# Kernel tuning notes

Measured on AMD Instinct MI355X. Metric: run time of the kernel, lower is better.

The kernel has to match this reference:

```python
import jax, jax.numpy as jnp
import numpy as np

N_NODES = 100000
N_NBRS = 16
D_IN = 512
D_EGO = 32
D_LOCAL = 32
D_GLOBAL = 32


def setup_inputs() -> dict:
    key = jax.random.key(0)
    ks = jax.random.split(key, 12)
    x = jax.random.uniform(ks[0], (N_NODES, D_IN), dtype=jnp.float32)
    # adj_list: row 0 = source (neighbor) node, row 1 = destination node.
    # score_local_sparse reshapes to [N, n, d_local], so dst must be each node
    # index repeated N_NBRS times, in order.
    src = jax.random.randint(ks[1], (N_NODES * N_NBRS,), 0, N_NODES, dtype=jnp.int32)
    dst = jnp.repeat(jnp.arange(N_NODES, dtype=jnp.int32), N_NBRS)
    adj_list = jnp.stack([src, dst], axis=0)
    return {
        "adj_list": adj_list,
        "x": x,
        "qk_ego_w": jax.random.normal(ks[2], (D_EGO, D_IN), dtype=jnp.float32) * 0.04,
        "v_ego_w": jax.random.normal(ks[3], (D_IN, D_EGO), dtype=jnp.float32) - 2.0,
        "q_local_w": jax.random.normal(ks[4], (D_LOCAL, D_IN), dtype=jnp.float32) / 10.0 - 2.0,
        "k_local_w": jax.random.normal(ks[5], (D_LOCAL, D_IN), dtype=jnp.float32) / 10.0 - 2.0,
        "v_local_w": jax.random.normal(ks[6], (D_IN, D_LOCAL), dtype=jnp.float32) / 10.0 - 2.0,
        "q_global_w": jax.random.normal(ks[7], (D_GLOBAL, D_IN), dtype=jnp.float32) / 10.0 - 2.0,
        "k_global_w": jax.random.normal(ks[8], (D_GLOBAL, D_IN), dtype=jnp.float32) / 10.0 - 2.0,
        "v_global_w": jax.random.normal(ks[9], (D_IN, D_GLOBAL), dtype=jnp.float32) / 10.0 - 2.0,
        "bias_b": jnp.zeros((1, D_IN), dtype=jnp.float32),
    }


def _nonneg(w):
    return jax.nn.elu(w) + 1.0


def _norm_nonneg(w):
    t = jax.nn.sigmoid(w)
    return t / t.sum()


def reference(adj_list, x, qk_ego_w, v_ego_w, q_local_w, k_local_w, v_local_w,
              q_global_w, k_global_w, v_global_w, bias_b):
    n_cells, d_in = x.shape
    inv = 1.0 / d_in
    inv2 = inv * inv

    # ego branch: plain linear, squared scores
    ego_emb = x @ qk_ego_w.T                      # [N, d_ego]
    ego_scores = (ego_emb * inv) ** 2             # [N, d_ego]

    # local branch: gather-based bilinear scores over k-NN graph
    q_loc = x @ _norm_nonneg(q_local_w).T         # [N, d_local]
    k_loc = x @ _nonneg(k_local_w).T              # [N, d_local]
    prod = q_loc[adj_list[1]] * k_loc[adj_list[0]]  # [E, d_local]
    n_nbr = prod.shape[0] // n_cells
    local_scores = prod.reshape(n_cells, n_nbr, -1) * inv2  # [N, n, d_local]
    exp_local = local_scores.sum(axis=1)          # [N, d_local] (sum over neighbors)

    # global branch: bilinear with mean cell x_bar
    x_bar = x.mean(axis=0, keepdims=True)         # [1, d_in]
    q_glob = x @ _norm_nonneg(q_global_w).T       # [N, d_global]
    k_glob = x_bar @ _nonneg(k_global_w).T        # [1, d_global]
    exp_global = q_glob * k_glob * inv2           # [N, d_global]

    sum_exp = (0.001
               + ego_scores.sum(axis=-1, keepdims=True)
               + exp_local.sum(axis=-1, keepdims=True)
               + exp_global.sum(axis=-1, keepdims=True))  # [N, 1]

    ego_res = (ego_scores / sum_exp) @ _nonneg(v_ego_w).T       # [N, d_out]
    local_res = (exp_local / sum_exp) @ _nonneg(v_local_w).T    # [N, d_out]
    global_res = (exp_global / sum_exp) @ _nonneg(v_global_w).T # [N, d_out]

    res = ego_res + local_res + global_res + (jax.nn.elu(bias_b) + 1.0)
    return res
```

## Files before the change

kernel.cpp:

```cpp
#include <hip/hip_runtime.h>
#include <hip/hip_bf16.h>
#include <math.h>

#define NNODES 100000
#define NNBRS  16
#define NBLK   ((NNODES + 127) / 128)
#define XCG    512

typedef short  s16x8 __attribute__((ext_vector_type(8)));
typedef ushort u16x8 __attribute__((ext_vector_type(8)));
typedef float  f32x4 __attribute__((ext_vector_type(4)));

__device__ __forceinline__ float nonneg_(float w) { return w > 0.f ? w + 1.f : __expf(w); }
__device__ __forceinline__ float sigmoid_(float w) { return 1.f / (1.f + __expf(-w)); }
__device__ __forceinline__ ushort f2b(float f) {
    unsigned u = __builtin_bit_cast(unsigned, f);
    return (ushort)((u + 0x7FFFu + ((u >> 16) & 1u)) >> 16);
}
__device__ __forceinline__ float b2f(ushort h) {
    return __builtin_bit_cast(float, (unsigned)h << 16);
}
__device__ __forceinline__ short fbh(float f) {
    __hip_bfloat16 h = __float2bfloat16(f);
    return __builtin_bit_cast(short, h);
}
__device__ __forceinline__ s16x8 cvt8(float4 lo, float4 hi) {
    s16x8 r;
    r[0] = fbh(lo.x); r[1] = fbh(lo.y); r[2] = fbh(lo.z); r[3] = fbh(lo.w);
    r[4] = fbh(hi.x); r[5] = fbh(hi.y); r[6] = fbh(hi.z); r[7] = fbh(hi.w);
    return r;
}

#define BAR() do {                                             \
    __builtin_amdgcn_sched_barrier(0);                         \
    asm volatile("s_waitcnt lgkmcnt(0)" ::: "memory");         \
    __builtin_amdgcn_sched_barrier(0);                         \
    __builtin_amdgcn_s_barrier();                              \
    __builtin_amdgcn_sched_barrier(0);                         \
} while (0)

__global__ __launch_bounds__(256) void k_sumsig(const float* __restrict__ qlw,
                                                const float* __restrict__ qgw,
                                                float* __restrict__ sums) {
    __shared__ float rr[8];
    const int tid = threadIdx.x, lane = tid & 63, wv = tid >> 6;
    const int base = blockIdx.x * 512;
    float s0 = sigmoid_(qlw[base + tid]) + sigmoid_(qlw[base + 256 + tid]);
    float s1 = sigmoid_(qgw[base + tid]) + sigmoid_(qgw[base + 256 + tid]);
#pragma unroll
    for (int o = 32; o > 0; o >>= 1) {
        s0 += __shfl_down(s0, o);
        s1 += __shfl_down(s1, o);
    }
    if (lane == 0) { rr[wv] = s0; rr[4 + wv] = s1; }
    __syncthreads();
    if (tid == 0) atomicAdd(&sums[0], rr[0] + rr[1] + rr[2] + rr[3]);
    if (tid == 1) atomicAdd(&sums[1], rr[4] + rr[5] + rr[6] + rr[7]);
}

__global__ __launch_bounds__(256) void k_xcast(const float* __restrict__ x,
                                               ushort* __restrict__ x_bf,
                                               float* __restrict__ xcs) {
    __shared__ float csred[4][512];
    const int t = threadIdx.x;
    const int NCH = (NNODES * 512) / 8;
    float a[8] = {0.f,0.f,0.f,0.f,0.f,0.f,0.f,0.f};
    for (int cid = blockIdx.x * 256 + t; cid < NCH; cid += XCG * 256 * 4) {
#pragma unroll
        for (int c4 = 0; c4 < 4; c4++) {
            int cc = cid + c4 * XCG * 256;
            if (cc < NCH) {
                size_t f = (size_t)cc * 8;
                float4 lo = *(const float4*)(x + f);
                float4 hi = *(const float4*)(x + f + 4);
                *(s16x8*)(x_bf + f) = cvt8(lo, hi);
                a[0]+=lo.x; a[1]+=lo.y; a[2]+=lo.z; a[3]+=lo.w;
                a[4]+=hi.x; a[5]+=hi.y; a[6]+=hi.z; a[7]+=hi.w;
            }
        }
    }
    const int c0 = (t * 8) & 511, slice = t >> 6;
#pragma unroll
    for (int j = 0; j < 8; j++) csred[slice][c0 + j] = a[j];
    __syncthreads();
    {
        const int c1 = t, c2 = t + 256;
        float s1 = csred[0][c1] + csred[1][c1] + csred[2][c1] + csred[3][c1];
        float s2 = csred[0][c2] + csred[1][c2] + csred[2][c2] + csred[3][c2];
        xcs[blockIdx.x * 512 + c1] = s1;
        xcs[blockIdx.x * 512 + c2] = s2;
    }
}

__global__ __launch_bounds__(256) void k_prep(const float* __restrict__ qk_ego,
                                              const float* __restrict__ qlw,
                                              const float* __restrict__ klw,
                                              const float* __restrict__ qgw,
                                              const float* __restrict__ ve,
                                              const float* __restrict__ vl,
                                              const float* __restrict__ vg,
                                              const float* __restrict__ bias_b,
                                              ushort* __restrict__ B1t,
                                              ushort* __restrict__ Vt,
                                              float* __restrict__ biasvec) {
    int idx = blockIdx.x * 256 + threadIdx.x;
    if (idx < 128 * 512) {
        int o = idx >> 9, k = idx & 511;
        float v;
        if (o < 32)       v = qk_ego[o * 512 + k];
        else if (o < 64)  v = sigmoid_(qlw[(o - 32) * 512 + k]);
        else if (o < 96)  v = nonneg_(klw[(o - 64) * 512 + k]);
        else              v = sigmoid_(qgw[(o - 96) * 512 + k]);
        B1t[idx] = f2b(v);
    } else if (idx < 128 * 512 + 512 * 96) {
        int j = idx - 128 * 512;
        int d = j / 96, e = j % 96;
        const float* src = (e < 32) ? ve : (e < 64 ? vl : vg);
        Vt[j] = f2b(nonneg_(src[d * 32 + (e & 31)]));
    } else if (idx < 128 * 512 + 512 * 96 + 512) {
        int d = idx - 128 * 512 - 512 * 96;
        float b = bias_b[d];
        biasvec[d] = (b > 0.f ? b + 1.f : __expf(b));
    }
}

__global__ __launch_bounds__(512) void k_proj(const ushort* __restrict__ x_bf,
                                              const ushort* __restrict__ B1t,
                                              ushort* __restrict__ ego_a,
                                              ushort* __restrict__ qloc_a,
                                              ushort* __restrict__ kloc_a,
                                              ushort* __restrict__ qglob_a) {
    __shared__ ushort Bs[128 * 128];
    const int t = threadIdx.x, lane = t & 63, w = t >> 6;
    const int lr = lane & 15, g = lane >> 4;
    const int row0 = blockIdx.x * 128;
    const int myrow = row0 + w * 16 + lr;
    const ushort* xr = x_bf + (size_t)(myrow < NNODES ? myrow : NNODES - 1) * 512
                       + g * 8;
    const char* B1tc = (const char*)B1t;

    uint4 bst[4];
#define BLOAD(seg) { _Pragma("unroll")                                        \
    for (int c = 0; c < 4; c++) {                                             \
        int l = c * 512 + t; int r = l >> 4; int sl = l & 15;                 \
        bst[c] = *(const uint4*)(B1tc + r * 1024 + (seg) * 256 + sl * 16);    \
    } }
#define BWRITE() { _Pragma("unroll")                                          \
    for (int c = 0; c < 4; c++) {                                             \
        int l = c * 512 + t; int r = l >> 4; int sl = l & 15;                 \
        *(uint4*)((char*)Bs + r * 256 + ((sl * 16) ^ ((r & 7) << 4))) =       \
            bst[c];                                                           \
    } }

    f32x4 acc[8];
#pragma unroll
    for (int n = 0; n < 8; n++) acc[n] = (f32x4){0.f, 0.f, 0.f, 0.f};

    s16x8 A0 = *(const s16x8*)(xr);
    s16x8 A1 = *(const s16x8*)(xr + 32);
    s16x8 A2 = *(const s16x8*)(xr + 64);
    s16x8 A3 = *(const s16x8*)(xr + 96);

    BLOAD(0)
    BWRITE()
    BAR();
    BLOAD(1)

#define ASTEP(AR)                                                             \
        af = AR;                                                              \
        if (s + 4 < 16) AR = *(const s16x8*)(xr + (s + 4) * 32);

#pragma unroll
    for (int s = 0; s < 16; s++) {
        const int st = s & 3, seg = s >> 2;
        if (st == 0 && seg > 0) {
            BAR();
            BWRITE();
            BAR();
            if (seg < 3) BLOAD(seg + 1)
        }
        s16x8 af;
        if (st == 0)      { ASTEP(A0) }
        else if (st == 1) { ASTEP(A1) }
        else if (st == 2) { ASTEP(A2) }
        else              { ASTEP(A3) }
#pragma unroll
        for (int n = 0; n < 8; n++) {
            s16x8 bf = *(const s16x8*)((const char*)Bs + (n * 16 + lr) * 256 +
                                       ((st * 64 + g * 16) ^ ((lr & 7) << 4)));
            acc[n] = __builtin_amdgcn_mfma_f32_16x16x32_bf16(af, bf, acc[n], 0, 0, 0);
        }
    }
#undef ASTEP
#undef BLOAD
#undef BWRITE

    __syncthreads();
    char* regn = (char*)Bs + w * 4096;
#pragma unroll
    for (int n = 0; n < 8; n++) {
        const int col = (n >> 1) * 32 + (n & 1) * 16 + lr;
#pragma unroll
        for (int i = 0; i < 4; i++) {
            int row = g * 4 + i;
            *(ushort*)(regn + row * 256 + ((col * 2) ^ ((row & 7) << 4))) =
                f2b(acc[n][i]);
        }
    }
    {
        const int rr = lane & 15, a2 = lane >> 4;
        uint4 v0 = *(const uint4*)(regn + rr * 256 + (( 0 + a2 * 64) ^ ((rr & 7) << 4)));
        uint4 v1 = *(const uint4*)(regn + rr * 256 + ((16 + a2 * 64) ^ ((rr & 7) << 4)));
        uint4 v2 = *(const uint4*)(regn + rr * 256 + ((32 + a2 * 64) ^ ((rr & 7) << 4)));
        uint4 v3 = *(const uint4*)(regn + rr * 256 + ((48 + a2 * 64) ^ ((rr & 7) << 4)));
        int grow = row0 + w * 16 + rr;
        if (grow < NNODES) {
            ushort* ap = (a2 == 0) ? ego_a : (a2 == 1) ? qloc_a
                        : (a2 == 2) ? kloc_a : qglob_a;
            uint4* dp = (uint4*)(ap + (size_t)grow * 32);
            dp[0] = v0; dp[1] = v1; dp[2] = v2; dp[3] = v3;
        }
    }
}

__global__ __launch_bounds__(256) void k_kredA(const float* __restrict__ xcs,
                                               float* __restrict__ csum2) {
    const int t = threadIdx.x, b = blockIdx.x;
    const float* base = xcs + (size_t)b * 8 * 512;
    float s1 = 0.f, s2 = 0.f;
#pragma unroll
    for (int r = 0; r < 8; r++) {
        s1 += base[r * 512 + t];
        s2 += base[r * 512 + 256 + t];
    }
    csum2[(size_t)b * 512 + t] = s1;
    csum2[(size_t)b * 512 + 256 + t] = s2;
}

__global__ __launch_bounds__(256) void k_kredB(const float* __restrict__ csum2,
                                               const float* __restrict__ kgw,
                                               float* __restrict__ kacc) {
    __shared__ float cs[512];
    const int t = threadIdx.x;
    float s0 = 0.f, s1 = 0.f;
    for (int b = 0; b < 64; b++) {
        s0 += csum2[(size_t)b * 512 + t];
        s1 += csum2[(size_t)b * 512 + 256 + t];
    }
    cs[t] = s0; cs[256 + t] = s1;
    __syncthreads();
    const int e = t >> 3, j = t & 7;
    float p = 0.f;
    for (int d = j * 64; d < j * 64 + 64; d++)
        p += cs[d] * nonneg_(kgw[e * 512 + d]);
    p += __shfl_xor(p, 1);
    p += __shfl_xor(p, 2);
    p += __shfl_xor(p, 4);
    if (j == 0) kacc[e] = p;
}

__global__ __launch_bounds__(256, 4) void k_fused(const ushort* __restrict__ ego_a,
                                                  const ushort* __restrict__ qloc_a,
                                                  const ushort* __restrict__ kloc_a,
                                                  const ushort* __restrict__ qglob_a,
                                                  const int* __restrict__ src,
                                                  const float* __restrict__ kacc,
                                                  const float* __restrict__ sums,
                                                  const ushort* __restrict__ Vt,
                                                  const float* __restrict__ biasvec,
                                                  float* __restrict__ out) {
    __shared__ float4 stg4[2048];
    char* stg = (char*)stg4;
    const int t = threadIdx.x, lane = t & 63, w = t >> 6;
    const int lr = lane & 15, g = lane >> 4;
    const int node = blockIdx.x * 64 + w * 16 + lr;
    const int nc = node < NNODES ? node : NNODES - 1;

    const float inv = 1.f / 512.f;
    const float inv2 = inv * inv;
    const float scl = inv2 / sums[0];
    const float scg = inv2 / sums[1] * (1.f / (float)NNODES);
    float kg[8];
    {
        float4 kg0 = *(const float4*)(kacc + g * 8);
        float4 kg1 = *(const float4*)(kacc + g * 8 + 4);
        kg[0]=kg0.x; kg[1]=kg0.y; kg[2]=kg0.z; kg[3]=kg0.w;
        kg[4]=kg1.x; kg[5]=kg1.y; kg[6]=kg1.z; kg[7]=kg1.w;
    }

    s16x8 p0, p1, p2;
    {
        u16x8 e8 = *(const u16x8*)(ego_a   + (size_t)nc * 32 + g * 8);
        u16x8 q8 = *(const u16x8*)(qloc_a  + (size_t)nc * 32 + g * 8);
        u16x8 g8 = *(const u16x8*)(qglob_a + (size_t)nc * 32 + g * 8);
        int4 si0 = *(const int4*)(src + (size_t)nc * 16);
        int4 si1 = *(const int4*)(src + (size_t)nc * 16 + 4);
        int4 si2 = *(const int4*)(src + (size_t)nc * 16 + 8);
        int4 si3 = *(const int4*)(src + (size_t)nc * 16 + 12);
        float ks[8] = {0.f,0.f,0.f,0.f,0.f,0.f,0.f,0.f};
#define GAT(sn) {                                                             \
        u16x8 kv = *(const u16x8*)(kloc_a + (size_t)(sn) * 32 + g * 8);       \
        _Pragma("unroll")                                                     \
        for (int j = 0; j < 8; j++) ks[j] += b2f(kv[j]);                      \
    }
        GAT(si0.x) GAT(si0.y) GAT(si0.z) GAT(si0.w)
        GAT(si1.x) GAT(si1.y) GAT(si1.z) GAT(si1.w)
        GAT(si2.x) GAT(si2.y) GAT(si2.z) GAT(si2.w)
        GAT(si3.x) GAT(si3.y) GAT(si3.z) GAT(si3.w)
#undef GAT
        float se[8], sl[8], sg[8];
        float tt = 0.f;
#pragma unroll
        for (int j = 0; j < 8; j++) {
            float e = b2f(e8[j]) * inv;
            se[j] = e * e;
            sl[j] = b2f(q8[j]) * ks[j] * scl;
            sg[j] = b2f(g8[j]) * kg[j] * scg;
            tt += se[j] + sl[j] + sg[j];
        }
        tt += __shfl_xor(tt, 16);
        tt += __shfl_xor(tt, 32);
        float is = 1.f / (0.001f + tt);
#pragma unroll
        for (int j = 0; j < 8; j++) {
            p0[j] = (short)f2b(se[j] * is);
            p1[j] = (short)f2b(sl[j] * is);
            p2[j] = (short)f2b(sg[j] * is);
        }
    }

    const int srow = w * 16 + lr;
    const int sxor = (srow & 7) << 4;
#pragma unroll
    for (int gi = 0; gi < 4; gi++) {
        if (gi) __syncthreads();
#pragma unroll
        for (int m2 = 0; m2 < 8; m2++) {
            const int m = gi * 8 + m2;
            const ushort* vp = Vt + (size_t)(m * 16 + lr) * 96 + g * 8;
            s16x8 a0 = *(const s16x8*)(vp);
            s16x8 a1 = *(const s16x8*)(vp + 32);
            s16x8 a2 = *(const s16x8*)(vp + 64);
            f32x4 dA = (f32x4){0.f,0.f,0.f,0.f};
            dA = __builtin_amdgcn_mfma_f32_16x16x32_bf16(a0, p0, dA, 0, 0, 0);
            dA = __builtin_amdgcn_mfma_f32_16x16x32_bf16(a1, p1, dA, 0, 0, 0);
            dA = __builtin_amdgcn_mfma_f32_16x16x32_bf16(a2, p2, dA, 0, 0, 0);
            float4 bb = *(const float4*)(biasvec + m * 16 + g * 4);
            float4 o4 = {dA[0]+bb.x, dA[1]+bb.y, dA[2]+bb.z, dA[3]+bb.w};
            *(float4*)(stg + srow * 512 + ((m2 * 64 + g * 16) ^ sxor)) = o4;
        }
        __syncthreads();
#pragma unroll
        for (int k = 0; k < 8; k++) {
            const int lin = k * 1024 + t * 4;
            const int row = lin >> 7, inrow = lin & 127;
            f32x4 v = *(const f32x4*)(stg + row * 512 +
                                      ((inrow * 4) ^ ((row & 7) << 4)));
            const int gnode = blockIdx.x * 64 + row;
            if (gnode < NNODES)
                __builtin_nontemporal_store(
                    v, (f32x4*)(out + (size_t)gnode * 512 + gi * 128 + inrow));
        }
    }
}

extern "C" void kernel_launch(void* const* d_in, const int* in_sizes, int n_in,
                              void* d_out, int out_size, void* d_ws, size_t ws_size,
                              hipStream_t stream) {
    (void)in_sizes; (void)n_in; (void)out_size; (void)ws_size;
    const int*   adj    = (const int*)d_in[0];
    const float* x      = (const float*)d_in[1];
    const float* qk_ego = (const float*)d_in[2];
    const float* v_ego  = (const float*)d_in[3];
    const float* qlw    = (const float*)d_in[4];
    const float* klw    = (const float*)d_in[5];
    const float* vl     = (const float*)d_in[6];
    const float* qgw    = (const float*)d_in[7];
    const float* kgw    = (const float*)d_in[8];
    const float* vg     = (const float*)d_in[9];
    const float* bias_b = (const float*)d_in[10];
    float* out = (float*)d_out;
    float* ws  = (float*)d_ws;

    float*  kacc    = ws;
    float*  sums    = ws + 32;
    float*  biasvec = ws + 64;
    ushort* B1t     = (ushort*)(ws + 1024);
    ushort* Vt      = (ushort*)(ws + 33792);
    ushort* ego_a   = (ushort*)(ws + 65536);
    ushort* qloc_a  = (ushort*)(ws + 65536 + 1600000);
    ushort* kloc_a  = (ushort*)(ws + 65536 + 3200000);
    ushort* qglob_a = (ushort*)(ws + 65536 + 4800000);
    float*  xcs     = ws + 6465536;
    ushort* x_bf    = (ushort*)(ws + 6750208);
    float*  csum2   = ws + 6750208 + 25600000;

    (void)hipMemsetAsync(sums, 0, 2 * sizeof(float), stream);
    k_sumsig<<<32, 256, 0, stream>>>(qlw, qgw, sums);
    k_xcast<<<XCG, 256, 0, stream>>>(x, x_bf, xcs);
    {
        int total = 128 * 512 + 512 * 96 + 512;
        k_prep<<<(total + 255) / 256, 256, 0, stream>>>(qk_ego, qlw, klw, qgw,
                                                        v_ego, vl, vg, bias_b,
                                                        B1t, Vt, biasvec);
    }
    k_proj<<<NBLK, 512, 0, stream>>>(x_bf, B1t, ego_a, qloc_a, kloc_a, qglob_a);
    k_kredA<<<64, 256, 0, stream>>>(xcs, csum2);
    k_kredB<<<1, 256, 0, stream>>>(csum2, kgw, kacc);
    k_fused<<<(NNODES + 63) / 64, 256, 0, stream>>>(ego_a, qloc_a, kloc_a, qglob_a,
                                                    adj, kacc, sums, Vt, biasvec, out);
}
```

Before: 179.8 us.

## Fuse fp32-to-bf16 cast and column sums into projection GEMM kernel

Removes the separate x cast kernel that wrote a full bf16 copy of x and reread it. The projection kernel now loads fp32 x directly, converts it to bf16 into a swizzled LDS tile, and accumulates per-block column sums for the mean. This drops one full write and read of the bf16 intermediate. In exchange it uses more LDS per block, adds extra shuffles, and stages A through LDS with extra barriers, which may lower occupancy.

```diff
diff --git a/kernel.cpp b/kernel.cpp
--- a/kernel.cpp
+++ b/kernel.cpp
@@ -5,7 +5,7 @@
 #define NNODES 100000
 #define NNBRS  16
 #define NBLK   ((NNODES + 127) / 128)
-#define XCG    512
+#define KRA    ((NBLK + 7) / 8)
 
 typedef short  s16x8 __attribute__((ext_vector_type(8)));
 typedef ushort u16x8 __attribute__((ext_vector_type(8)));
@@ -56,40 +56,6 @@
     __syncthreads();
     if (tid == 0) atomicAdd(&sums[0], rr[0] + rr[1] + rr[2] + rr[3]);
     if (tid == 1) atomicAdd(&sums[1], rr[4] + rr[5] + rr[6] + rr[7]);
-}
-
-__global__ __launch_bounds__(256) void k_xcast(const float* __restrict__ x,
-                                               ushort* __restrict__ x_bf,
-                                               float* __restrict__ xcs) {
-    __shared__ float csred[4][512];
-    const int t = threadIdx.x;
-    const int NCH = (NNODES * 512) / 8;
-    float a[8] = {0.f,0.f,0.f,0.f,0.f,0.f,0.f,0.f};
-    for (int cid = blockIdx.x * 256 + t; cid < NCH; cid += XCG * 256 * 4) {
-#pragma unroll
-        for (int c4 = 0; c4 < 4; c4++) {
-            int cc = cid + c4 * XCG * 256;
-            if (cc < NCH) {
-                size_t f = (size_t)cc * 8;
-                float4 lo = *(const float4*)(x + f);
-                float4 hi = *(const float4*)(x + f + 4);
-                *(s16x8*)(x_bf + f) = cvt8(lo, hi);
-                a[0]+=lo.x; a[1]+=lo.y; a[2]+=lo.z; a[3]+=lo.w;
-                a[4]+=hi.x; a[5]+=hi.y; a[6]+=hi.z; a[7]+=hi.w;
-            }
-        }
-    }
-    const int c0 = (t * 8) & 511, slice = t >> 6;
-#pragma unroll
-    for (int j = 0; j < 8; j++) csred[slice][c0 + j] = a[j];
-    __syncthreads();
-    {
-        const int c1 = t, c2 = t + 256;
-        float s1 = csred[0][c1] + csred[1][c1] + csred[2][c1] + csred[3][c1];
-        float s2 = csred[0][c2] + csred[1][c2] + csred[2][c2] + csred[3][c2];
-        xcs[blockIdx.x * 512 + c1] = s1;
-        xcs[blockIdx.x * 512 + c2] = s2;
-    }
 }
 
 __global__ __launch_bounds__(256) void k_prep(const float* __restrict__ qk_ego,
@@ -124,19 +90,21 @@
     }
 }
 
-__global__ __launch_bounds__(512) void k_proj(const ushort* __restrict__ x_bf,
-                                              const ushort* __restrict__ B1t,
-                                              ushort* __restrict__ ego_a,
-                                              ushort* __restrict__ qloc_a,
-                                              ushort* __restrict__ kloc_a,
-                                              ushort* __restrict__ qglob_a) {
+__global__ __launch_bounds__(512, 2) void k_projx(const float* __restrict__ x,
+                                                  const ushort* __restrict__ B1t,
+                                                  ushort* __restrict__ ego_a,
+                                                  ushort* __restrict__ qloc_a,
+                                                  ushort* __restrict__ kloc_a,
+                                                  ushort* __restrict__ qglob_a,
+                                                  float* __restrict__ xcs) {
+    __shared__ ushort As[128 * 128];
     __shared__ ushort Bs[128 * 128];
+    __shared__ float  cs[8][512];
     const int t = threadIdx.x, lane = t & 63, w = t >> 6;
     const int lr = lane & 15, g = lane >> 4;
     const int row0 = blockIdx.x * 128;
-    const int myrow = row0 + w * 16 + lr;
-    const ushort* xr = x_bf + (size_t)(myrow < NNODES ? myrow : NNODES - 1) * 512
-                       + g * 8;
+    const int arow_ = t >> 4;
+    const int acol_ = (t & 15) * 8;
     const char* B1tc = (const char*)B1t;
 
     uint4 bst[4];
@@ -152,50 +120,80 @@
             bst[c];                                                           \
     } }
 
+    float4 al0[4], al1[4];
+#define ALOAD(seg) { _Pragma("unroll")                                        \
+    for (int p = 0; p < 4; p++) {                                             \
+        int rr = p * 32 + arow_;                                              \
+        int grow = row0 + rr; if (grow > NNODES - 1) grow = NNODES - 1;       \
+        const float* sp = x + (size_t)grow * 512 + (seg) * 128 + acol_;       \
+        al0[p] = *(const float4*)(sp);                                        \
+        al1[p] = *(const float4*)(sp + 4);                                    \
+    } }
+#define AWRITE(seg) {                                                         \
+    float a8[8] = {0.f,0.f,0.f,0.f,0.f,0.f,0.f,0.f};                          \
+    _Pragma("unroll")                                                         \
+    for (int p = 0; p < 4; p++) {                                             \
+        int rr = p * 32 + arow_;                                              \
+        if (row0 + rr < NNODES) {                                             \
+            a8[0]+=al0[p].x; a8[1]+=al0[p].y; a8[2]+=al0[p].z; a8[3]+=al0[p].w;\
+            a8[4]+=al1[p].x; a8[5]+=al1[p].y; a8[6]+=al1[p].z; a8[7]+=al1[p].w;\
+        }                                                                     \
+        *(s16x8*)((char*)As + rr * 256 + ((acol_ * 2) ^ ((rr & 7) << 4))) =   \
+            cvt8(al0[p], al1[p]);                                             \
+    }                                                                         \
+    _Pragma("unroll")                                                         \
+    for (int j = 0; j < 8; j++) {                                             \
+        a8[j] += __shfl_xor(a8[j], 16);                                       \
+        a8[j] += __shfl_xor(a8[j], 32);                                       \
+    }                                                                         \
+    if ((lane >> 4) == 0) { _Pragma("unroll")                                 \
+        for (int j = 0; j < 8; j++)                                           \
+            cs[w][(seg) * 128 + lr * 8 + j] = a8[j];                          \
+    } }
+
     f32x4 acc[8];
 #pragma unroll
     for (int n = 0; n < 8; n++) acc[n] = (f32x4){0.f, 0.f, 0.f, 0.f};
 
-    s16x8 A0 = *(const s16x8*)(xr);
-    s16x8 A1 = *(const s16x8*)(xr + 32);
-    s16x8 A2 = *(const s16x8*)(xr + 64);
-    s16x8 A3 = *(const s16x8*)(xr + 96);
-
+    ALOAD(0)
     BLOAD(0)
+    AWRITE(0)
     BWRITE()
     BAR();
-    BLOAD(1)
-
-#define ASTEP(AR)                                                             \
-        af = AR;                                                              \
-        if (s + 4 < 16) AR = *(const s16x8*)(xr + (s + 4) * 32);
-
-#pragma unroll
-    for (int s = 0; s < 16; s++) {
-        const int st = s & 3, seg = s >> 2;
-        if (st == 0 && seg > 0) {
+
+#pragma unroll
+    for (int seg = 0; seg < 4; seg++) {
+        if (seg < 3) { ALOAD(seg + 1) BLOAD(seg + 1) }
+#pragma unroll
+        for (int st = 0; st < 4; st++) {
+            const int ar = w * 16 + lr;
+            s16x8 af = *(const s16x8*)((const char*)As + ar * 256 +
+                                       ((st * 64 + g * 16) ^ ((ar & 7) << 4)));
+#pragma unroll
+            for (int n = 0; n < 8; n++) {
+                s16x8 bf = *(const s16x8*)((const char*)Bs + (n * 16 + lr) * 256 +
+                                           ((st * 64 + g * 16) ^ ((lr & 7) << 4)));
+                acc[n] = __builtin_amdgcn_mfma_f32_16x16x32_bf16(af, bf, acc[n], 0, 0, 0);
+            }
+        }
+        if (seg < 3) {
             BAR();
-            BWRITE();
+            AWRITE(seg + 1)
+            BWRITE()
             BAR();
-            if (seg < 3) BLOAD(seg + 1)
-        }
-        s16x8 af;
-        if (st == 0)      { ASTEP(A0) }
-        else if (st == 1) { ASTEP(A1) }
-        else if (st == 2) { ASTEP(A2) }
-        else              { ASTEP(A3) }
-#pragma unroll
-        for (int n = 0; n < 8; n++) {
-            s16x8 bf = *(const s16x8*)((const char*)Bs + (n * 16 + lr) * 256 +
-                                       ((st * 64 + g * 16) ^ ((lr & 7) << 4)));
-            acc[n] = __builtin_amdgcn_mfma_f32_16x16x32_bf16(af, bf, acc[n], 0, 0, 0);
-        }
-    }
-#undef ASTEP
+        }
+    }
+#undef ALOAD
+#undef AWRITE
 #undef BLOAD
 #undef BWRITE
 
     __syncthreads();
+    if (t < 512) {
+        float s = cs[0][t] + cs[1][t] + cs[2][t] + cs[3][t]
+                + cs[4][t] + cs[5][t] + cs[6][t] + cs[7][t];
+        xcs[(size_t)blockIdx.x * 512 + t] = s;
+    }
     char* regn = (char*)Bs + w * 4096;
 #pragma unroll
     for (int n = 0; n < 8; n++) {
@@ -226,12 +224,14 @@
 __global__ __launch_bounds__(256) void k_kredA(const float* __restrict__ xcs,
                                                float* __restrict__ csum2) {
     const int t = threadIdx.x, b = blockIdx.x;
-    const float* base = xcs + (size_t)b * 8 * 512;
     float s1 = 0.f, s2 = 0.f;
 #pragma unroll
     for (int r = 0; r < 8; r++) {
-        s1 += base[r * 512 + t];
-        s2 += base[r * 512 + 256 + t];
+        int row = b * 8 + r;
+        if (row < NBLK) {
+            s1 += xcs[(size_t)row * 512 + t];
+            s2 += xcs[(size_t)row * 512 + 256 + t];
+        }
     }
     csum2[(size_t)b * 512 + t] = s1;
     csum2[(size_t)b * 512 + 256 + t] = s2;
@@ -243,7 +243,7 @@
     __shared__ float cs[512];
     const int t = threadIdx.x;
     float s0 = 0.f, s1 = 0.f;
-    for (int b = 0; b < 64; b++) {
+    for (int b = 0; b < KRA; b++) {
         s0 += csum2[(size_t)b * 512 + t];
         s1 += csum2[(size_t)b * 512 + 256 + t];
     }
@@ -392,20 +392,18 @@
     ushort* kloc_a  = (ushort*)(ws + 65536 + 3200000);
     ushort* qglob_a = (ushort*)(ws + 65536 + 4800000);
     float*  xcs     = ws + 6465536;
-    ushort* x_bf    = (ushort*)(ws + 6750208);
-    float*  csum2   = ws + 6750208 + 25600000;
+    float*  csum2   = ws + 6465536 + 400384;
 
     (void)hipMemsetAsync(sums, 0, 2 * sizeof(float), stream);
     k_sumsig<<<32, 256, 0, stream>>>(qlw, qgw, sums);
-    k_xcast<<<XCG, 256, 0, stream>>>(x, x_bf, xcs);
     {
         int total = 128 * 512 + 512 * 96 + 512;
         k_prep<<<(total + 255) / 256, 256, 0, stream>>>(qk_ego, qlw, klw, qgw,
                                                         v_ego, vl, vg, bias_b,
                                                         B1t, Vt, biasvec);
     }
-    k_proj<<<NBLK, 512, 0, stream>>>(x_bf, B1t, ego_a, qloc_a, kloc_a, qglob_a);
-    k_kredA<<<64, 256, 0, stream>>>(xcs, csum2);
+    k_projx<<<NBLK, 512, 0, stream>>>(x, B1t, ego_a, qloc_a, kloc_a, qglob_a, xcs);
+    k_kredA<<<KRA, 256, 0, stream>>>(xcs, csum2);
     k_kredB<<<1, 256, 0, stream>>>(csum2, kgw, kacc);
     k_fused<<<(NNODES + 63) / 64, 256, 0, stream>>>(ego_a, qloc_a, kloc_a, qglob_a,
                                                     adj, kacc, sums, Vt, biasvec, out);
```

Result: faster. 162.2 us, median of 2 (-9.7%).
